# Optimization experiments

Measured on AMD Instinct MI355X. Metric: run time of the kernel, lower is better.

## Reference

```python
import jax, jax.numpy as jnp
import numpy as np

B, N, H, NH = 2, 1024, 1024, 16  # batch, seq per branch, hidden, heads


def setup_inputs() -> dict:
    key = jax.random.key(0)
    k1, k2, k3, k4 = jax.random.split(key, 4)
    x = jax.random.normal(k1, (B, N, H), jnp.float32)
    x2 = jax.random.normal(k2, (B, N, H), jnp.float32)
    w_qkv = jax.random.normal(k3, (3 * H, H), jnp.float32) * 0.02  # nn.Linear(H, 3H), no bias
    w_out = jax.random.normal(k4, (H, H), jnp.float32) * 0.02
    b_out = jnp.zeros((H,), jnp.float32)
    return {"x": x, "x2": x2, "w_qkv": w_qkv, "w_out": w_out, "b_out": b_out, "num_heads": NH}


def _qkv_split(x, w_qkv, nh):
    # qkv Linear then Rearrange 'b n (qkv l d) -> qkv b l n d'
    b, n, h = x.shape
    d = h // nh
    qkv = x @ w_qkv.T                                    # [b, n, 3h]
    qkv = qkv.reshape(b, n, 3, nh, d).transpose(2, 0, 3, 1, 4)  # [3, b, nh, n, d]
    return qkv[0], qkv[1], qkv[2]


def reference(x, x2, w_qkv, w_out, b_out, num_heads):
    nh = num_heads
    d = x.shape[-1] // nh
    scale = float(d) ** -0.5
    q, k, v = _qkv_split(x, w_qkv, nh)
    q2, k2, v2 = _qkv_split(x2, w_qkv, nh)
    # cross-branch concat along seq dim
    q = jnp.concatenate([q, q2], axis=2)
    k = jnp.concatenate([k, k2], axis=2)
    v = jnp.concatenate([v, v2], axis=2)
    att = jax.nn.softmax(jnp.einsum('bhxd,bhyd->bhxy', q, k) * scale, axis=-1)  # [b,nh,2N,2N]
    o = jnp.einsum('bhxy,bhyd->bhxd', att, v)            # [b,nh,2N,d]
    o1, o2 = jnp.split(o, 2, axis=2)

    def proj(o):
        b, h, n, dd = o.shape
        o = o.transpose(0, 2, 1, 3).reshape(b, n, h * dd)  # 'b h l d -> b l (h d)'
        return o @ w_out.T + b_out

    return proj(o1), proj(o2)
```

## Files before the change

### kernel.cpp

```cpp
#include <hip/hip_runtime.h>
#include <hip/hip_bf16.h>

#define NB      2
#define NSEQ    1024
#define S2      2048
#define HDIM    1024
#define NHEADS  16
#define DHEAD   64
#define Q_SCALE 0.18033688011112042f

typedef unsigned short ushort_t;
typedef __attribute__((ext_vector_type(8))) short short8;
typedef __attribute__((ext_vector_type(4))) float f32x4;
typedef __attribute__((ext_vector_type(16))) float f32x16;

__device__ __forceinline__ ushort_t f2bf(float f) {
    union { float f; unsigned int u; } c; c.f = f;
    unsigned int u = c.u;
    u += 0x7FFFu + ((u >> 16) & 1u);
    return (ushort_t)(u >> 16);
}

__device__ __forceinline__ unsigned pack_bf16x2(float a, float b) {
    union { __hip_bfloat162 h; unsigned u; } cv;
    cv.h = __float22bfloat162_rn(float2{a, b});
    return cv.u;
}

__global__ __launch_bounds__(256) void cvt_all(
    const float* __restrict__ x, const float* __restrict__ x2,
    const float* __restrict__ wqkv, const float* __restrict__ wout,
    ushort_t* __restrict__ Xb, ushort_t* __restrict__ Wqb, ushort_t* __restrict__ Wob)
{
    int b = blockIdx.x;
    const float* s; ushort_t* d; int i;
    if (b < 2048)      { s = x;    d = Xb;            i = b * 256 + threadIdx.x; }
    else if (b < 4096) { s = x2;   d = Xb + 2097152;  i = (b - 2048) * 256 + threadIdx.x; }
    else if (b < 7168) { s = wqkv; d = Wqb;           i = (b - 4096) * 256 + threadIdx.x; }
    else               { s = wout; d = Wob;           i = (b - 7168) * 256 + threadIdx.x; }
    float4 v = ((const float4*)s)[i];
    ushort4 o; o.x = f2bf(v.x); o.y = f2bf(v.y); o.z = f2bf(v.z); o.w = f2bf(v.w);
    ((ushort4*)d)[i] = o;
}

__global__ __launch_bounds__(256) void qkv_gemm_mfma(
    const ushort_t* __restrict__ Xb, const ushort_t* __restrict__ Wqb,
    ushort_t* __restrict__ Qb, ushort_t* __restrict__ Kb, ushort_t* __restrict__ Vtb)
{
    __shared__ ushort_t As[2 * 128 * 32];
    __shared__ ushort_t Bs[2 * 128 * 32];
    __shared__ float    Sc[4][16 * 20];
    const int t = threadIdx.x;
    const int lane = t & 63, quad = lane >> 4, l15 = lane & 15;
    const int w = t >> 6;
    const int wm = (w >> 1) * 64, wn = (w & 1) * 64;
    const int r0 = blockIdx.y * 128, c0 = blockIdx.x * 128;

    const int g_chunk = (lane & 3) ^ ((lane >> 3) & 3);
    const int srow_lo = w * 16 + (lane >> 2);

    auto stage = [&](int k0, int buf) {
        #pragma unroll
        for (int p = 0; p < 2; ++p) {
            int row = srow_lo + p * 64;
            const ushort_t* gpA = Xb  + (size_t)(r0 + row) * HDIM + k0 + g_chunk * 8;
            const ushort_t* gpB = Wqb + (size_t)(c0 + row) * HDIM + k0 + g_chunk * 8;
            ushort_t* lpA = As + buf * 4096 + p * 2048 + w * 512;
            ushort_t* lpB = Bs + buf * 4096 + p * 2048 + w * 512;
            __builtin_amdgcn_global_load_lds(
                (const __attribute__((address_space(1))) void*)gpA,
                (__attribute__((address_space(3))) void*)lpA, 16, 0, 0);
            __builtin_amdgcn_global_load_lds(
                (const __attribute__((address_space(1))) void*)gpB,
                (__attribute__((address_space(3))) void*)lpB, 16, 0, 0);
        }
    };

    f32x4 acc[4][4];
    #pragma unroll
    for (int i = 0; i < 4; ++i)
        #pragma unroll
        for (int j = 0; j < 4; ++j) acc[i][j] = (f32x4){0.f, 0.f, 0.f, 0.f};

    stage(0, 0);
    stage(32, 1);
    __syncthreads();

    const int sw = (l15 >> 1) & 3;
    for (int it = 0; it < 32; ++it) {
        const ushort_t* a = As + (it & 1) * 4096;
        const ushort_t* b = Bs + (it & 1) * 4096;
        short8 af[4], bf[4];
        #pragma unroll
        for (int mi = 0; mi < 4; ++mi) {
            int ra = wm + mi * 16 + l15;
            af[mi] = *(const short8*)(a + ra * 32 + ((quad ^ sw) * 8));
        }
        #pragma unroll
        for (int ni = 0; ni < 4; ++ni) {
            int rb = wn + ni * 16 + l15;
            bf[ni] = *(const short8*)(b + rb * 32 + ((quad ^ sw) * 8));
        }
        #pragma unroll
        for (int mi = 0; mi < 4; ++mi)
            #pragma unroll
            for (int ni = 0; ni < 4; ++ni)
                acc[mi][ni] = __builtin_amdgcn_mfma_f32_16x16x32_bf16(af[mi], bf[ni], acc[mi][ni], 0, 0, 0);
        __syncthreads();
        if (it < 30) stage((it + 2) * 32, it & 1);
    }

    const int branch = r0 >> 11;
    const int bb     = (r0 & 2047) >> 10;
    const int qi     = c0 >> 10;
    float* sc = &Sc[w][0];

    if (qi == 2) {
        #pragma unroll
        for (int mi = 0; mi < 4; ++mi) {
            int sbase = branch * NSEQ + (r0 & 1023) + wm + mi * 16 + quad * 4;
            #pragma unroll
            for (int ni = 0; ni < 4; ++ni) {
                int cc = (c0 & 1023) + wn + ni * 16;
                int h  = cc >> 6;
                int dd = (cc & 63) + l15;
                ushort4 pv;
                pv.x = f2bf(acc[mi][ni][0]); pv.y = f2bf(acc[mi][ni][1]);
                pv.z = f2bf(acc[mi][ni][2]); pv.w = f2bf(acc[mi][ni][3]);
                *(ushort4*)(Vtb + ((size_t)(bb * NHEADS + h) * DHEAD + dd) * S2 + sbase) = pv;
            }
        }
    } else {
        const float qsc = (qi == 0) ? Q_SCALE : 1.0f;
        ushort_t* base = (qi ? Kb : Qb);
        const int row = lane >> 2, ch = lane & 3;
        #pragma unroll
        for (int mi = 0; mi < 4; ++mi) {
            int sb = branch * NSEQ + (r0 & 1023) + wm + mi * 16;
            #pragma unroll
            for (int ni = 0; ni < 4; ++ni) {
                int cc = (c0 & 1023) + wn + ni * 16;
                int h  = cc >> 6;
                int db = cc & 63;
                #pragma unroll
                for (int reg = 0; reg < 4; ++reg)
                    sc[(quad * 4 + reg) * 20 + l15] = acc[mi][ni][reg] * qsc;
                float4 v = *(const float4*)&sc[row * 20 + ch * 4];
                uint2 pk;
                pk.x = pack_bf16x2(v.x, v.y);
                pk.y = pack_bf16x2(v.z, v.w);
                *(uint2*)(base + ((size_t)(bb * NHEADS + h) * S2 + sb + row) * DHEAD + db + ch * 4) = pk;
            }
        }
    }
}

__global__ __launch_bounds__(256) void attn_mfma(
    const ushort_t* __restrict__ Qb, const ushort_t* __restrict__ Kb,
    const ushort_t* __restrict__ Vtb, ushort_t* __restrict__ Ob)
{
    __shared__ ushort_t Ks[2][64 * 64];
    __shared__ ushort_t Vs[2][64 * 64];

    const int t = threadIdx.x, lane = t & 63, w = t >> 6;
    const int l31 = lane & 31, hi = lane >> 5;
    const int bh = blockIdx.z * NHEADS + blockIdx.y;
    const int r0 = blockIdx.x * 128;
    const ushort_t* Qh  = Qb  + (size_t)bh * S2 * DHEAD;
    const ushort_t* Kh  = Kb  + (size_t)bh * S2 * DHEAD;
    const ushort_t* Vth = Vtb + (size_t)bh * DHEAD * S2;

    const int slot = lane & 7;
    const int rsub = lane >> 3;
    auto prefetch = [&](int kt_, int buf_) {
        #pragma unroll
        for (int c = 0; c < 2; ++c) {
            int row = w * 16 + c * 8 + rsub;
            int g   = slot ^ (row & 7);
            const ushort_t* gpK = Kh  + (size_t)(kt_ * 64 + row) * DHEAD + g * 8;
            const ushort_t* gpV = Vth + (size_t)row * S2 + kt_ * 64 + g * 8;
            ushort_t* lpK = &Ks[buf_][w * 1024 + c * 512];
            ushort_t* lpV = &Vs[buf_][w * 1024 + c * 512];
            __builtin_amdgcn_global_load_lds(
                (const __attribute__((address_space(1))) void*)gpK,
                (__attribute__((address_space(3))) void*)lpK, 16, 0, 0);
            __builtin_amdgcn_global_load_lds(
                (const __attribute__((address_space(1))) void*)gpV,
                (__attribute__((address_space(3))) void*)lpV, 16, 0, 0);
        }
    };

    short8 aq[4];
    {
        const ushort_t* qp = Qh + (size_t)(r0 + 32 * w + l31) * DHEAD + hi * 8;
        #pragma unroll
        for (int sd = 0; sd < 4; ++sd) aq[sd] = *(const short8*)(qp + sd * 16);
    }

    const int s7 = l31 & 7;
    int offA[4];
    #pragma unroll
    for (int s = 0; s < 4; ++s)
        offA[s] = (l31 * 64 + (((s * 2 + hi) ^ s7) * 8)) * 2;

    f32x16 oacc0, oacc1;
    #pragma unroll
    for (int i = 0; i < 16; ++i) { oacc0[i] = 0.f; oacc1[i] = 0.f; }
    float la0 = 0.f, la1 = 0.f, la2 = 0.f, la3 = 0.f;

    prefetch(0, 0);
    prefetch(1, 1);
    __syncthreads();

    for (int kt = 0; kt < S2 / 64; ++kt) {
        const char* kb = (const char*)&Ks[kt & 1][0];
        const char* vb = (const char*)&Vs[kt & 1][0];

        f32x16 s0, s1;
        #pragma unroll
        for (int i = 0; i < 16; ++i) { s0[i] = 0.f; s1[i] = 0.f; }
        __builtin_amdgcn_s_setprio(1);
        #pragma unroll
        for (int sd = 0; sd < 4; ++sd) {
            short8 k0 = *(const short8*)(kb + offA[sd]);
            short8 k1 = *(const short8*)(kb + offA[sd] + 4096);
            s0 = __builtin_amdgcn_mfma_f32_32x32x16_bf16(k0, aq[sd], s0, 0, 0, 0);
            s1 = __builtin_amdgcn_mfma_f32_32x32x16_bf16(k1, aq[sd], s1, 0, 0, 0);
        }
        __builtin_amdgcn_s_setprio(0);

        unsigned pw[4][4];
        #pragma unroll
        for (int half = 0; half < 2; ++half) {
            float p[8], q[8];
            #pragma unroll
            for (int j = 0; j < 8; ++j) {
                p[j] = __builtin_exp2f(s0[half * 8 + j]);
                q[j] = __builtin_exp2f(s1[half * 8 + j]);
            }
            la0 += p[0] + p[4]; la1 += p[1] + p[5];
            la2 += p[2] + p[6]; la3 += p[3] + p[7];
            la0 += q[0] + q[4]; la1 += q[1] + q[5];
            la2 += q[2] + q[6]; la3 += q[3] + q[7];

            unsigned a0 = pack_bf16x2(p[0], p[1]), b0 = pack_bf16x2(p[2], p[3]);
            unsigned c0 = pack_bf16x2(p[4], p[5]), d0 = pack_bf16x2(p[6], p[7]);
            asm("v_permlane32_swap_b32 %0, %1" : "+v"(a0), "+v"(c0));
            asm("v_permlane32_swap_b32 %0, %1" : "+v"(b0), "+v"(d0));
            pw[half][0] = a0; pw[half][1] = b0; pw[half][2] = c0; pw[half][3] = d0;

            unsigned a1 = pack_bf16x2(q[0], q[1]), b1 = pack_bf16x2(q[2], q[3]);
            unsigned c1 = pack_bf16x2(q[4], q[5]), d1 = pack_bf16x2(q[6], q[7]);
            asm("v_permlane32_swap_b32 %0, %1" : "+v"(a1), "+v"(c1));
            asm("v_permlane32_swap_b32 %0, %1" : "+v"(b1), "+v"(d1));
            pw[2 + half][0] = a1; pw[2 + half][1] = b1; pw[2 + half][2] = c1; pw[2 + half][3] = d1;
        }

        __builtin_amdgcn_s_setprio(1);
        #pragma unroll
        for (int sk = 0; sk < 4; ++sk) {
            union { unsigned u[4]; short8 s8; } pa;
            pa.u[0] = pw[sk][0]; pa.u[1] = pw[sk][1];
            pa.u[2] = pw[sk][2]; pa.u[3] = pw[sk][3];
            short8 v0 = *(const short8*)(vb + offA[sk]);
            short8 v1 = *(const short8*)(vb + offA[sk] + 4096);
            oacc0 = __builtin_amdgcn_mfma_f32_32x32x16_bf16(pa.s8, v0, oacc0, 0, 0, 0);
            oacc1 = __builtin_amdgcn_mfma_f32_32x32x16_bf16(pa.s8, v1, oacc1, 0, 0, 0);
        }
        __builtin_amdgcn_s_setprio(0);

        __syncthreads();
        if (kt + 2 < S2 / 64) prefetch(kt + 2, kt & 1);
    }

    float l = (la0 + la1) + (la2 + la3);
    l += __shfl_xor(l, 32);
    const float inv = 1.0f / l;

    ushort_t* obase = Ob + (size_t)bh * S2 * DHEAD;
    #pragma unroll
    for (int r = 0; r < 16; ++r) {
        const int ql = (r & 3) + 8 * (r >> 2) + 4 * hi;
        const float iv = __shfl(inv, ql);
        const size_t rowoff = (size_t)(r0 + 32 * w + ql) * DHEAD;
        obase[rowoff + l31]      = f2bf(oacc0[r] * iv);
        obase[rowoff + 32 + l31] = f2bf(oacc1[r] * iv);
    }
}

__global__ __launch_bounds__(256) void proj_gemm_mfma(
    const ushort_t* __restrict__ Ob, const ushort_t* __restrict__ Wob,
    const float* __restrict__ Bo, float* __restrict__ Out)
{
    __shared__ ushort_t As[2 * 128 * 32];
    __shared__ ushort_t Bs[2 * 64 * 32];
    __shared__ float    Sc[4][16 * 20];
    const int t = threadIdx.x;
    const int lane = t & 63, quad = lane >> 4, l15 = lane & 15;
    const int w = t >> 6;
    const int wm = (w >> 1) * 64, wn = (w & 1) * 32;
    const int r0 = blockIdx.y * 128, c0 = blockIdx.x * 64;
    const int branch = r0 >> 11, bb = (r0 & 2047) >> 10;

    const int g_chunk = (lane & 3) ^ ((lane >> 3) & 3);
    const int srow_lo = w * 16 + (lane >> 2);

    auto stage = [&](int k0, int buf) {
        int h = k0 >> 6, off = k0 & 63;
        const ushort_t* gpB = Wob + (size_t)(c0 + srow_lo) * HDIM + k0 + g_chunk * 8;
        ushort_t* lpB = Bs + buf * 2048 + w * 512;
        __builtin_amdgcn_global_load_lds(
            (const __attribute__((address_space(1))) void*)gpB,
            (__attribute__((address_space(3))) void*)lpB, 16, 0, 0);
        #pragma unroll
        for (int p = 0; p < 2; ++p) {
            int row = srow_lo + p * 64;
            int s = branch * NSEQ + (r0 & 1023) + row;
            const ushort_t* gpA = Ob + ((size_t)(bb * NHEADS + h) * S2 + s) * DHEAD + off + g_chunk * 8;
            ushort_t* lpA = As + buf * 4096 + p * 2048 + w * 512;
            __builtin_amdgcn_global_load_lds(
                (const __attribute__((address_space(1))) void*)gpA,
                (__attribute__((address_space(3))) void*)lpA, 16, 0, 0);
        }
    };

    f32x4 acc[4][2];
    #pragma unroll
    for (int i = 0; i < 4; ++i)
        #pragma unroll
        for (int j = 0; j < 2; ++j) acc[i][j] = (f32x4){0.f, 0.f, 0.f, 0.f};

    stage(0, 0);
    stage(32, 1);
    __syncthreads();

    const int sw = (l15 >> 1) & 3;
    for (int it = 0; it < 32; ++it) {
        const ushort_t* a = As + (it & 1) * 4096;
        const ushort_t* b = Bs + (it & 1) * 2048;
        short8 af[4], bf[2];
        #pragma unroll
        for (int mi = 0; mi < 4; ++mi) {
            int ra = wm + mi * 16 + l15;
            af[mi] = *(const short8*)(a + ra * 32 + ((quad ^ sw) * 8));
        }
        #pragma unroll
        for (int ni = 0; ni < 2; ++ni) {
            int rb = wn + ni * 16 + l15;
            bf[ni] = *(const short8*)(b + rb * 32 + ((quad ^ sw) * 8));
        }
        #pragma unroll
        for (int mi = 0; mi < 4; ++mi)
            #pragma unroll
            for (int ni = 0; ni < 2; ++ni)
                acc[mi][ni] = __builtin_amdgcn_mfma_f32_16x16x32_bf16(af[mi], bf[ni], acc[mi][ni], 0, 0, 0);
        __syncthreads();
        if (it < 30) stage((it + 2) * 32, it & 1);
    }

    float* sc = &Sc[w][0];
    const int row = lane >> 2, ch = lane & 3;
    #pragma unroll
    for (int mi = 0; mi < 4; ++mi) {
        int rb0 = r0 + wm + mi * 16;
        #pragma unroll
        for (int ni = 0; ni < 2; ++ni) {
            int cb = c0 + wn + ni * 16;
            #pragma unroll
            for (int reg = 0; reg < 4; ++reg)
                sc[(quad * 4 + reg) * 20 + l15] = acc[mi][ni][reg];
            float4 v = *(const float4*)&sc[row * 20 + ch * 4];
            float4 bias = *(const float4*)&Bo[cb + ch * 4];
            v.x += bias.x; v.y += bias.y; v.z += bias.z; v.w += bias.w;
            *(float4*)&Out[(size_t)(rb0 + row) * HDIM + cb + ch * 4] = v;
        }
    }
}

extern "C" void kernel_launch(void* const* d_in, const int* in_sizes, int n_in,
                              void* d_out, int out_size, void* d_ws, size_t ws_size,
                              hipStream_t stream) {
    const float* x    = (const float*)d_in[0];
    const float* x2   = (const float*)d_in[1];
    const float* wqkv = (const float*)d_in[2];
    const float* wout = (const float*)d_in[3];
    const float* bout = (const float*)d_in[4];
    float* out = (float*)d_out;

    char* ws = (char*)d_ws;
    ushort_t* Xb  = (ushort_t*)(ws);
    ushort_t* Wqb = (ushort_t*)(ws + (8u  << 20));
    ushort_t* Wob = (ushort_t*)(ws + (14u << 20));
    ushort_t* Qb  = (ushort_t*)(ws + (16u << 20));
    ushort_t* Kb  = (ushort_t*)(ws + (24u << 20));
    ushort_t* Vtb = (ushort_t*)(ws + (32u << 20));
    ushort_t* Ob  = (ushort_t*)(ws + (40u << 20));

    cvt_all<<<8192, 256, 0, stream>>>(x, x2, wqkv, wout, Xb, Wqb, Wob);
    qkv_gemm_mfma<<<dim3(24, 32), 256, 0, stream>>>(Xb, Wqb, Qb, Kb, Vtb);
    attn_mfma<<<dim3(S2 / 128, NHEADS, NB), 256, 0, stream>>>(Qb, Kb, Vtb, Ob);
    proj_gemm_mfma<<<dim3(16, 32), 256, 0, stream>>>(Ob, Wob, bout, out);
}
```

Baseline: 212.7 us.

## Triple-buffer K/V tiles with vmcnt waits and remap attention block grid

Result: no change. 209.8 us (-1.4%).

```diff
diff --git a/kernel.cpp b/kernel.cpp
--- a/kernel.cpp
+++ b/kernel.cpp
@@ -159,13 +159,17 @@
     const ushort_t* __restrict__ Qb, const ushort_t* __restrict__ Kb,
     const ushort_t* __restrict__ Vtb, ushort_t* __restrict__ Ob)
 {
-    __shared__ ushort_t Ks[2][64 * 64];
-    __shared__ ushort_t Vs[2][64 * 64];
+    __shared__ ushort_t Ks[3 * 64 * 64];
+    __shared__ ushort_t Vs[3 * 64 * 64];
 
     const int t = threadIdx.x, lane = t & 63, w = t >> 6;
     const int l31 = lane & 31, hi = lane >> 5;
-    const int bh = blockIdx.z * NHEADS + blockIdx.y;
-    const int r0 = blockIdx.x * 128;
+
+    const int id  = blockIdx.x;
+    const int j   = id >> 3;
+    const int bh  = ((j & 3) << 3) | (id & 7);
+    const int r0  = (j >> 2) * 128;
+
     const ushort_t* Qh  = Qb  + (size_t)bh * S2 * DHEAD;
     const ushort_t* Kh  = Kb  + (size_t)bh * S2 * DHEAD;
     const ushort_t* Vth = Vtb + (size_t)bh * DHEAD * S2;
@@ -179,8 +183,8 @@
             int g   = slot ^ (row & 7);
             const ushort_t* gpK = Kh  + (size_t)(kt_ * 64 + row) * DHEAD + g * 8;
             const ushort_t* gpV = Vth + (size_t)row * S2 + kt_ * 64 + g * 8;
-            ushort_t* lpK = &Ks[buf_][w * 1024 + c * 512];
-            ushort_t* lpV = &Vs[buf_][w * 1024 + c * 512];
+            ushort_t* lpK = &Ks[buf_ * 4096 + w * 1024 + c * 512];
+            ushort_t* lpV = &Vs[buf_ * 4096 + w * 1024 + c * 512];
             __builtin_amdgcn_global_load_lds(
                 (const __attribute__((address_space(1))) void*)gpK,
                 (__attribute__((address_space(3))) void*)lpK, 16, 0, 0);
@@ -210,11 +214,16 @@
 
     prefetch(0, 0);
     prefetch(1, 1);
-    __syncthreads();
-
+
+    int bi = 0;
     for (int kt = 0; kt < S2 / 64; ++kt) {
-        const char* kb = (const char*)&Ks[kt & 1][0];
-        const char* vb = (const char*)&Vs[kt & 1][0];
+        if (kt < S2 / 64 - 1) asm volatile("s_waitcnt vmcnt(4)" ::: "memory");
+        else                  asm volatile("s_waitcnt vmcnt(0)" ::: "memory");
+        __builtin_amdgcn_s_barrier();
+        __builtin_amdgcn_sched_barrier(0);
+
+        const char* kb = (const char*)Ks + bi * 8192;
+        const char* vb = (const char*)Vs + bi * 8192;
 
         f32x16 s0, s1;
         #pragma unroll
@@ -234,9 +243,9 @@
         for (int half = 0; half < 2; ++half) {
             float p[8], q[8];
             #pragma unroll
-            for (int j = 0; j < 8; ++j) {
-                p[j] = __builtin_exp2f(s0[half * 8 + j]);
-                q[j] = __builtin_exp2f(s1[half * 8 + j]);
+            for (int jj = 0; jj < 8; ++jj) {
+                p[jj] = __builtin_exp2f(s0[half * 8 + jj]);
+                q[jj] = __builtin_exp2f(s1[half * 8 + jj]);
             }
             la0 += p[0] + p[4]; la1 += p[1] + p[5];
             la2 += p[2] + p[6]; la3 += p[3] + p[7];
@@ -269,8 +278,11 @@
         }
         __builtin_amdgcn_s_setprio(0);
 
-        __syncthreads();
-        if (kt + 2 < S2 / 64) prefetch(kt + 2, kt & 1);
+        if (kt + 2 < S2 / 64) {
+            int pb = bi + 2; if (pb >= 3) pb -= 3;
+            prefetch(kt + 2, pb);
+        }
+        bi = (bi == 2) ? 0 : bi + 1;
     }
 
     float l = (la0 + la1) + (la2 + la3);
@@ -398,6 +410,6 @@
 
     cvt_all<<<8192, 256, 0, stream>>>(x, x2, wqkv, wout, Xb, Wqb, Wob);
     qkv_gemm_mfma<<<dim3(24, 32), 256, 0, stream>>>(Xb, Wqb, Qb, Kb, Vtb);
-    attn_mfma<<<dim3(S2 / 128, NHEADS, NB), 256, 0, stream>>>(Qb, Kb, Vtb, Ob);
+    attn_mfma<<<512, 256, 0, stream>>>(Qb, Kb, Vtb, Ob);
     proj_gemm_mfma<<<dim3(16, 32), 256, 0, stream>>>(Ob, Wob, bout, out);
 }
```
